# Optimization experiments

Measured on AMD Instinct MI355X. Metric: run time of the kernel, lower is better.

## Reference

```python
import jax, jax.numpy as jnp
import numpy as np

HEADS = 4
OUT_CH = 64
NEG_SLOPE = 0.2  # PyG GATConv default negative_slope


def setup_inputs() -> dict:
    key = jax.random.key(0)
    k1, k2, k3, k4, k5, k6 = jax.random.split(key, 6)
    N, E, IN_CH = 50000, 800000, 128
    x = jax.random.normal(k1, (N, IN_CH), dtype=jnp.float32)
    edge_index = jax.random.randint(k2, (2, E), 0, N, dtype=jnp.int64)
    # Learned parameters (glorot-style init)
    s_w = (6.0 / (IN_CH + HEADS * OUT_CH)) ** 0.5
    W = jax.random.uniform(k3, (IN_CH, HEADS * OUT_CH), minval=-s_w, maxval=s_w, dtype=jnp.float32)
    s_a = (6.0 / (1 + OUT_CH)) ** 0.5
    att_src = jax.random.uniform(k4, (HEADS, OUT_CH), minval=-s_a, maxval=s_a, dtype=jnp.float32)
    att_dst = jax.random.uniform(k5, (HEADS, OUT_CH), minval=-s_a, maxval=s_a, dtype=jnp.float32)
    bias = jnp.zeros((HEADS * OUT_CH,), dtype=jnp.float32)
    return {"x": x, "W": W, "att_src": att_src, "att_dst": att_dst, "bias": bias, "edge_index": edge_index}


def reference(x, W, att_src, att_dst, bias, edge_index):
    # Faithful GATConv (PyG defaults: add_self_loops=True, concat=True, eval mode => no dropout)
    N = x.shape[0]
    loops = jnp.arange(N, dtype=edge_index.dtype)
    src = jnp.concatenate([edge_index[0], loops])  # message source j
    dst = jnp.concatenate([edge_index[1], loops])  # message target i

    xp = (x @ W).reshape(N, HEADS, OUT_CH)          # [N, H, C]
    a_src = jnp.einsum('nhc,hc->nh', xp, att_src)   # [N, H]
    a_dst = jnp.einsum('nhc,hc->nh', xp, att_dst)   # [N, H]

    alpha = jax.nn.leaky_relu(a_src[src] + a_dst[dst], NEG_SLOPE)  # [E', H]
    # segment softmax over incoming edges of each target node
    amax = jax.ops.segment_max(alpha, dst, num_segments=N)
    ex = jnp.exp(alpha - jax.lax.stop_gradient(amax)[dst])
    denom = jax.ops.segment_sum(ex, dst, num_segments=N)
    coef = ex / denom[dst]                           # [E', H]

    msg = xp[src] * coef[:, :, None]                 # [E', H, C]
    out = jax.ops.segment_sum(msg, dst, num_segments=N)  # [N, H, C]
    return out.reshape(N, HEADS * OUT_CH) + bias
```

## Files before the change

kernel.cpp:

```cpp
#include <hip/hip_runtime.h>

#define HEADS 4
#define OUTC 64
#define INC 128
#define HC 256
#define NEG 0.2f

typedef __attribute__((ext_vector_type(8))) short bf16x8;
typedef __attribute__((ext_vector_type(4))) float f32x4;

static __device__ __forceinline__ float bf2f(unsigned short u){
  unsigned int x = ((unsigned int)u) << 16;
  return __uint_as_float(x);
}
static __device__ __forceinline__ unsigned short f2bf(float f){
  unsigned int x = __float_as_uint(f);
  unsigned int lsb = (x >> 16) & 1u;
  x += 0x7fffu + lsb;
  return (unsigned short)(x >> 16);
}
static __device__ __forceinline__ void split8(float4 a, float4 b, bf16x8& hi, bf16x8& lo){
  float v[8] = {a.x, a.y, a.z, a.w, b.x, b.y, b.z, b.w};
  #pragma unroll
  for (int i = 0; i < 8; ++i){
    unsigned short h = f2bf(v[i]);
    hi[i] = (short)h;
    lo[i] = (short)f2bf(v[i] - bf2f(h));
  }
}

__global__ void k_conv_e_hist(const int* __restrict__ ei,
                              int* __restrict__ srcc, int* __restrict__ dstc,
                              int* __restrict__ pos, int* __restrict__ deg, int E){
  int e = blockIdx.x * 256 + threadIdx.x;
  bool valid = (e < E);
  int ee = valid ? e : 0;
  int hiw = ei[2 * ee + 1];
  bool hz = valid ? (hiw == 0) : true;
  unsigned long long mask = __ballot(hz);
  bool i64 = (mask == ~0ULL);
  int s, d;
  if (i64){ s = ei[2 * ee]; d = ei[2 * (size_t)E + 2 * ee]; }
  else    { s = ei[ee];     d = ei[(size_t)E + ee]; }
  if (valid){
    srcc[e] = s; dstc[e] = d;
    pos[e] = atomicAdd(&deg[d], 1);
  }
}

__global__ void k_split_w(const float* __restrict__ W, unsigned short* __restrict__ Wthi,
                          unsigned short* __restrict__ Wtlo){
  int t = blockIdx.x * 256 + threadIdx.x;
  int k = t >> 8, n = t & 255;
  float v = W[t];
  unsigned short hi = f2bf(v);
  Wthi[n * INC + k] = hi;
  Wtlo[n * INC + k] = f2bf(v - bf2f(hi));
}

__global__ __launch_bounds__(256) void k_gemm_fused(const float* __restrict__ X,
    const unsigned short* __restrict__ Wthi, const unsigned short* __restrict__ Wtlo,
    const float* __restrict__ att_src, const float* __restrict__ att_dst,
    unsigned short* __restrict__ XPh, float* __restrict__ a_src, float* __restrict__ a_dst,
    int N){
  int w = threadIdx.x >> 6, lane = threadIdx.x & 63;
  int m0 = blockIdx.x * 64;
  int quad = lane >> 4;
  int l15 = lane & 15;
  int colg[4];
  #pragma unroll
  for (int t = 0; t < 4; ++t) colg[t] = w * 64 + t * 16 + l15;

  bool rv[4]; int rowr[4];
  #pragma unroll
  for (int rt = 0; rt < 4; ++rt){
    rv[rt] = (m0 + rt * 16) < N;
    rowr[rt] = rv[rt] ? (m0 + rt * 16 + l15) : 0;
  }

  f32x4 acc[4][4];
  #pragma unroll
  for (int rt = 0; rt < 4; ++rt)
    #pragma unroll
    for (int t = 0; t < 4; ++t) acc[rt][t] = (f32x4){0.f, 0.f, 0.f, 0.f};

  #pragma unroll
  for (int kk = 0; kk < 4; ++kk){
    float4 va[4], vb[4];
    #pragma unroll
    for (int rt = 0; rt < 4; ++rt){
      const float* xr = X + (size_t)rowr[rt] * INC + kk * 32 + quad * 8;
      va[rt] = *(const float4*)xr;
      vb[rt] = *(const float4*)(xr + 4);
    }
    bf16x8 bh[4], bl[4];
    #pragma unroll
    for (int t = 0; t < 4; ++t){
      size_t bo = (size_t)colg[t] * INC + kk * 32 + quad * 8;
      bh[t] = *(const bf16x8*)(Wthi + bo);
      bl[t] = *(const bf16x8*)(Wtlo + bo);
    }
    bf16x8 ah[4], al[4];
    #pragma unroll
    for (int rt = 0; rt < 4; ++rt) split8(va[rt], vb[rt], ah[rt], al[rt]);
    #pragma unroll
    for (int rt = 0; rt < 4; ++rt){
      #pragma unroll
      for (int t = 0; t < 4; ++t){
        acc[rt][t] = __builtin_amdgcn_mfma_f32_16x16x32_bf16(ah[rt], bh[t], acc[rt][t], 0, 0, 0);
        acc[rt][t] = __builtin_amdgcn_mfma_f32_16x16x32_bf16(ah[rt], bl[t], acc[rt][t], 0, 0, 0);
        acc[rt][t] = __builtin_amdgcn_mfma_f32_16x16x32_bf16(al[rt], bh[t], acc[rt][t], 0, 0, 0);
      }
    }
  }

  #pragma unroll
  for (int rt = 0; rt < 4; ++rt){
    if (!rv[rt]) continue;
    #pragma unroll
    for (int t = 0; t < 4; ++t){
      #pragma unroll
      for (int r = 0; r < 4; ++r){
        XPh[(size_t)(m0 + rt * 16 + quad * 4 + r) * HC + colg[t]] = f2bf(acc[rt][t][r]);
      }
    }
  }

  float as[4], ad[4];
  #pragma unroll
  for (int t = 0; t < 4; ++t){
    as[t] = att_src[colg[t]];
    ad[t] = att_dst[colg[t]];
  }
  #pragma unroll
  for (int rt = 0; rt < 4; ++rt){
    if (!rv[rt]) continue;
    float ps[4], pd[4];
    #pragma unroll
    for (int r = 0; r < 4; ++r){
      ps[r] = acc[rt][0][r] * as[0] + acc[rt][1][r] * as[1]
            + acc[rt][2][r] * as[2] + acc[rt][3][r] * as[3];
      pd[r] = acc[rt][0][r] * ad[0] + acc[rt][1][r] * ad[1]
            + acc[rt][2][r] * ad[2] + acc[rt][3][r] * ad[3];
    }
    #pragma unroll
    for (int msk = 1; msk < 16; msk <<= 1){
      #pragma unroll
      for (int r = 0; r < 4; ++r){
        ps[r] += __shfl_xor(ps[r], msk, 64);
        pd[r] += __shfl_xor(pd[r], msk, 64);
      }
    }
    if (l15 == 0){
      #pragma unroll
      for (int r = 0; r < 4; ++r){
        int n = m0 + rt * 16 + quad * 4 + r;
        a_src[n * HEADS + w] = ps[r];
        a_dst[n * HEADS + w] = pd[r];
      }
    }
  }
}

__global__ __launch_bounds__(256) void k_scan1(const int* __restrict__ deg,
                                               int* __restrict__ out,
                                               int* __restrict__ bsum, int N){
  __shared__ int tsum[256];
  int t = threadIdx.x;
  int base = blockIdx.x * 1024 + t * 4;
  int v[4]; int s = 0;
  #pragma unroll
  for (int k = 0; k < 4; ++k){ int i = base + k; v[k] = (i < N) ? deg[i] : 0; s += v[k]; }
  tsum[t] = s;
  __syncthreads();
  for (int off = 1; off < 256; off <<= 1){
    int x = (t >= off) ? tsum[t - off] : 0;
    __syncthreads();
    tsum[t] += x;
    __syncthreads();
  }
  int excl = tsum[t] - s;
  if (t == 255) bsum[blockIdx.x] = tsum[255];
  int run = excl;
  #pragma unroll
  for (int k = 0; k < 4; ++k){ int i = base + k; if (i < N) out[i] = run; run += v[k]; }
}

__global__ __launch_bounds__(256) void k_scan23(int* __restrict__ rowstart,
                                                const int* __restrict__ bsum,
                                                int N, int E){
  int lane = threadIdx.x & 63;
  int partial = 0;
  for (int i = lane; i < blockIdx.x; i += 64) partial += bsum[i];
  #pragma unroll
  for (int msk = 32; msk; msk >>= 1) partial += __shfl_xor(partial, msk, 64);
  int base = blockIdx.x * 1024 + threadIdx.x * 4;
  #pragma unroll
  for (int k = 0; k < 4; ++k){ int i = base + k; if (i < N) rowstart[i] += partial; }
  if (blockIdx.x == 0 && threadIdx.x == 0) rowstart[N] = E;
}

__global__ void k_scatter(const int* __restrict__ srcc, const int* __restrict__ dstc,
                          const int* __restrict__ pos, const int* __restrict__ rowstart,
                          int* __restrict__ csr, int E){
  int e = blockIdx.x * 256 + threadIdx.x;
  if (e < E){
    int d = dstc[e];
    csr[rowstart[d] + pos[e]] = srcc[e];
  }
}

__global__ __launch_bounds__(256) void k_fused(const unsigned short* __restrict__ XPh,
    const float* __restrict__ a_src, const float* __restrict__ a_dst,
    const int* __restrict__ rowstart, const int* __restrict__ csr,
    const float* __restrict__ bias, float* __restrict__ out, int N){
  __shared__ float sh[4][64][4];
  int w = threadIdx.x >> 6, lane = threadIdx.x & 63;
  int n = blockIdx.x * 4 + w;
  bool alive = (n < N);
  if (!alive) n = 0;
  int r0 = rowstart[n], r1 = rowstart[n + 1];
  int deg = r1 - r0;
  int total = deg + 1;
  int h = lane >> 4;
  float4 ad4 = *(const float4*)&a_dst[n * HEADS];
  bool fast = (total <= 64);
  int jv = n;
  float msel = 0.f, inv_sel = 0.f;

  if (fast){
    if (lane < deg) jv = csr[r0 + lane];
    float l0 = -1e30f, l1 = -1e30f, l2 = -1e30f, l3 = -1e30f;
    if (lane < total){
      float4 a4 = *(const float4*)&a_src[jv * HEADS];
      l0 = a4.x + ad4.x; l0 = (l0 > 0.f) ? l0 : NEG * l0;
      l1 = a4.y + ad4.y; l1 = (l1 > 0.f) ? l1 : NEG * l1;
      l2 = a4.z + ad4.z; l2 = (l2 > 0.f) ? l2 : NEG * l2;
      l3 = a4.w + ad4.w; l3 = (l3 > 0.f) ? l3 : NEG * l3;
    }
    float p0 = __expf(l0), p1 = __expf(l1), p2 = __expf(l2), p3 = __expf(l3);
    float s0 = p0, s1 = p1, s2 = p2, s3 = p3;
    #pragma unroll
    for (int msk = 32; msk; msk >>= 1){
      s0 += __shfl_xor(s0, msk, 64);
      s1 += __shfl_xor(s1, msk, 64);
      s2 += __shfl_xor(s2, msk, 64);
      s3 += __shfl_xor(s3, msk, 64);
    }
    if (lane < total){
      sh[w][lane][0] = p0 / s0;
      sh[w][lane][1] = p1 / s1;
      sh[w][lane][2] = p2 / s2;
      sh[w][lane][3] = p3 / s3;
    }
  } else {
    float m[4] = {-1e30f, -1e30f, -1e30f, -1e30f};
    float s[4] = {0.f, 0.f, 0.f, 0.f};
    float adArr[4] = {ad4.x, ad4.y, ad4.z, ad4.w};
    for (int e = lane; e < total; e += 64){
      int j = (e < deg) ? csr[r0 + e] : n;
      float4 a4 = *(const float4*)&a_src[j * HEADS];
      float aa[4] = {a4.x, a4.y, a4.z, a4.w};
      #pragma unroll
      for (int hh = 0; hh < 4; ++hh){
        float l = aa[hh] + adArr[hh];
        l = (l > 0.f) ? l : NEG * l;
        if (l > m[hh]){ s[hh] = s[hh] * __expf(m[hh] - l) + 1.f; m[hh] = l; }
        else            s[hh] += __expf(l - m[hh]);
      }
    }
    #pragma unroll
    for (int hh = 0; hh < 4; ++hh){
      float mm = m[hh], ss = s[hh];
      #pragma unroll
      for (int msk = 32; msk; msk >>= 1){
        float m2 = __shfl_xor(mm, msk, 64);
        float s2 = __shfl_xor(ss, msk, 64);
        float M = fmaxf(mm, m2);
        float ns = 0.f;
        if (mm > -1e29f) ns += ss * __expf(mm - M);
        if (m2 > -1e29f) ns += s2 * __expf(m2 - M);
        mm = M; ss = ns;
      }
      m[hh] = mm; s[hh] = ss;
    }
    msel    = (h == 0) ? m[0] : (h == 1) ? m[1] : (h == 2) ? m[2] : m[3];
    inv_sel = 1.f / ((h == 0) ? s[0] : (h == 1) ? s[1] : (h == 2) ? s[2] : s[3]);
  }

  __syncthreads();

  float a0 = 0.f, a1 = 0.f, a2 = 0.f, a3 = 0.f;
  const unsigned short* xb = XPh + lane * 4;
  if (fast){
    int e = 0;
    for (; e + 8 <= total; e += 8){
      int jj[8]; float cf[8]; ushort4 xv[8];
      #pragma unroll
      for (int q = 0; q < 8; ++q){
        jj[q] = __builtin_amdgcn_readlane(jv, e + q);
        cf[q] = sh[w][e + q][h];
      }
      #pragma unroll
      for (int q = 0; q < 8; ++q) xv[q] = *(const ushort4*)(xb + (size_t)jj[q] * HC);
      #pragma unroll
      for (int q = 0; q < 8; ++q){
        a0 += cf[q] * bf2f(xv[q].x); a1 += cf[q] * bf2f(xv[q].y);
        a2 += cf[q] * bf2f(xv[q].z); a3 += cf[q] * bf2f(xv[q].w);
      }
    }
    for (; e < total; ++e){
      int j = __builtin_amdgcn_readlane(jv, e);
      float c = sh[w][e][h];
      ushort4 xv = *(const ushort4*)(xb + (size_t)j * HC);
      a0 += c * bf2f(xv.x); a1 += c * bf2f(xv.y); a2 += c * bf2f(xv.z); a3 += c * bf2f(xv.w);
    }
  } else {
    float adh = (h == 0) ? ad4.x : (h == 1) ? ad4.y : (h == 2) ? ad4.z : ad4.w;
    for (int e = 0; e < total; ++e){
      int j = (e < deg) ? csr[r0 + e] : n;
      float4 a4 = *(const float4*)&a_src[j * HEADS];
      float ah = (h == 0) ? a4.x : (h == 1) ? a4.y : (h == 2) ? a4.z : a4.w;
      float l = ah + adh;
      l = (l > 0.f) ? l : NEG * l;
      float c = __expf(l - msel) * inv_sel;
      ushort4 xv = *(const ushort4*)(xb + (size_t)j * HC);
      a0 += c * bf2f(xv.x); a1 += c * bf2f(xv.y); a2 += c * bf2f(xv.z); a3 += c * bf2f(xv.w);
    }
  }
  if (alive){
    float4 b4 = *(const float4*)&bias[lane * 4];
    float4 r; r.x = a0 + b4.x; r.y = a1 + b4.y; r.z = a2 + b4.z; r.w = a3 + b4.w;
    *(float4*)&out[(size_t)n * HC + lane * 4] = r;
  }
}

extern "C" void kernel_launch(void* const* d_in, const int* in_sizes, int n_in,
                              void* d_out, int out_size, void* d_ws, size_t ws_size,
                              hipStream_t stream){
  const float* x       = (const float*)d_in[0];
  const float* W       = (const float*)d_in[1];
  const float* att_src = (const float*)d_in[2];
  const float* att_dst = (const float*)d_in[3];
  const float* bias    = (const float*)d_in[4];
  const int*   ei      = (const int*)d_in[5];
  int N = in_sizes[0] / INC;
  int E = in_sizes[5] / 2;

  char* p = (char*)d_ws;
  auto alloc = [&](size_t bytes)->char*{
    char* r = p; p += (bytes + 255) & ~(size_t)255; return r;
  };
  unsigned short* Wthi = (unsigned short*)alloc((size_t)INC * HC * 2);
  unsigned short* Wtlo = (unsigned short*)alloc((size_t)INC * HC * 2);
  unsigned short* XPh  = (unsigned short*)alloc((size_t)N * HC * 2);
  float* aSrc          = (float*)alloc((size_t)N * HEADS * 4);
  float* aDst          = (float*)alloc((size_t)N * HEADS * 4);
  int* deg             = (int*)alloc((size_t)N * 4);
  int* rowstart        = (int*)alloc(((size_t)N + 1) * 4);
  int* srcc            = (int*)alloc((size_t)E * 4);
  int* dstc            = (int*)alloc((size_t)E * 4);
  int* pos             = (int*)alloc((size_t)E * 4);
  int* csr             = (int*)alloc((size_t)E * 4);
  int* bsum            = (int*)alloc(256 * 4);

  hipMemsetAsync(deg, 0, (size_t)N * 4, stream);
  k_conv_e_hist<<<(E + 255) / 256, 256, 0, stream>>>(ei, srcc, dstc, pos, deg, E);

  k_split_w<<<(INC * HC) / 256, 256, 0, stream>>>(W, Wthi, Wtlo);
  k_gemm_fused<<<(N + 63) / 64, 256, 0, stream>>>(x, Wthi, Wtlo, att_src, att_dst,
                                                  XPh, aSrc, aDst, N);

  int nb = (N + 1023) / 1024;
  k_scan1<<<nb, 256, 0, stream>>>(deg, rowstart, bsum, N);
  k_scan23<<<nb, 256, 0, stream>>>(rowstart, bsum, N, E);
  k_scatter<<<(E + 255) / 256, 256, 0, stream>>>(srcc, dstc, pos, rowstart, csr, E);

  k_fused<<<(N + 3) / 4, 256, 0, stream>>>(XPh, aSrc, aDst, rowstart, csr, bias,
                                           (float*)d_out, N);
}
```

Measured before the change: 249.4 us.

## Merge preprocessing kernels, share split X tiles via LDS, use nontemporal output stores

Folds the W split kernel and the edge conversion/histogram kernel into one launch, which saves a kernel launch. In the GEMM, each wave now loads and splits only its own 16 rows of X and shares the bf16 hi/lo parts through LDS. Previously every wave redundantly loaded and split all 64 rows, so this trades redundant global loads and conversion ALU work for extra barriers. It also drops a __syncthreads in the aggregation kernel and writes the output with nontemporal stores to avoid polluting the cache.

```diff
diff --git a/kernel.cpp b/kernel.cpp
--- a/kernel.cpp
+++ b/kernel.cpp
@@ -29,10 +29,22 @@
   }
 }
 
-__global__ void k_conv_e_hist(const int* __restrict__ ei,
-                              int* __restrict__ srcc, int* __restrict__ dstc,
-                              int* __restrict__ pos, int* __restrict__ deg, int E){
-  int e = blockIdx.x * 256 + threadIdx.x;
+#define SPLITB 128
+
+__global__ void k_pre(const float* __restrict__ W, unsigned short* __restrict__ Wthi,
+                      unsigned short* __restrict__ Wtlo, const int* __restrict__ ei,
+                      int* __restrict__ srcc, int* __restrict__ dstc,
+                      int* __restrict__ pos, int* __restrict__ deg, int E){
+  if (blockIdx.x < SPLITB){
+    int t = blockIdx.x * 256 + threadIdx.x;
+    int k = t >> 8, n = t & 255;
+    float v = W[t];
+    unsigned short hi = f2bf(v);
+    Wthi[n * INC + k] = hi;
+    Wtlo[n * INC + k] = f2bf(v - bf2f(hi));
+    return;
+  }
+  int e = (blockIdx.x - SPLITB) * 256 + threadIdx.x;
   bool valid = (e < E);
   int ee = valid ? e : 0;
   int hiw = ei[2 * ee + 1];
@@ -48,21 +60,13 @@
   }
 }
 
-__global__ void k_split_w(const float* __restrict__ W, unsigned short* __restrict__ Wthi,
-                          unsigned short* __restrict__ Wtlo){
-  int t = blockIdx.x * 256 + threadIdx.x;
-  int k = t >> 8, n = t & 255;
-  float v = W[t];
-  unsigned short hi = f2bf(v);
-  Wthi[n * INC + k] = hi;
-  Wtlo[n * INC + k] = f2bf(v - bf2f(hi));
-}
-
 __global__ __launch_bounds__(256) void k_gemm_fused(const float* __restrict__ X,
     const unsigned short* __restrict__ Wthi, const unsigned short* __restrict__ Wtlo,
     const float* __restrict__ att_src, const float* __restrict__ att_dst,
     unsigned short* __restrict__ XPh, float* __restrict__ a_src, float* __restrict__ a_dst,
     int N){
+  __shared__ unsigned short shi[64][40];
+  __shared__ unsigned short slo[64][40];
   int w = threadIdx.x >> 6, lane = threadIdx.x & 63;
   int m0 = blockIdx.x * 64;
   int quad = lane >> 4;
@@ -71,12 +75,10 @@
   #pragma unroll
   for (int t = 0; t < 4; ++t) colg[t] = w * 64 + t * 16 + l15;
 
-  bool rv[4]; int rowr[4];
-  #pragma unroll
-  for (int rt = 0; rt < 4; ++rt){
-    rv[rt] = (m0 + rt * 16) < N;
-    rowr[rt] = rv[rt] ? (m0 + rt * 16 + l15) : 0;
-  }
+  bool rv[4];
+  #pragma unroll
+  for (int rt = 0; rt < 4; ++rt) rv[rt] = (m0 + rt * 16) < N;
+  int myrow = rv[w] ? (m0 + w * 16 + l15) : 0;
 
   f32x4 acc[4][4];
   #pragma unroll
@@ -86,13 +88,9 @@
 
   #pragma unroll
   for (int kk = 0; kk < 4; ++kk){
-    float4 va[4], vb[4];
-    #pragma unroll
-    for (int rt = 0; rt < 4; ++rt){
-      const float* xr = X + (size_t)rowr[rt] * INC + kk * 32 + quad * 8;
-      va[rt] = *(const float4*)xr;
-      vb[rt] = *(const float4*)(xr + 4);
-    }
+    const float* xr = X + (size_t)myrow * INC + kk * 32 + quad * 8;
+    float4 va = *(const float4*)xr;
+    float4 vb = *(const float4*)(xr + 4);
     bf16x8 bh[4], bl[4];
     #pragma unroll
     for (int t = 0; t < 4; ++t){
@@ -100,9 +98,18 @@
       bh[t] = *(const bf16x8*)(Wthi + bo);
       bl[t] = *(const bf16x8*)(Wtlo + bo);
     }
+    bf16x8 ah1, al1;
+    split8(va, vb, ah1, al1);
+    if (kk) __syncthreads();
+    *(bf16x8*)&shi[w * 16 + l15][quad * 8] = ah1;
+    *(bf16x8*)&slo[w * 16 + l15][quad * 8] = al1;
+    __syncthreads();
     bf16x8 ah[4], al[4];
     #pragma unroll
-    for (int rt = 0; rt < 4; ++rt) split8(va[rt], vb[rt], ah[rt], al[rt]);
+    for (int rt = 0; rt < 4; ++rt){
+      ah[rt] = *(const bf16x8*)&shi[rt * 16 + l15][quad * 8];
+      al[rt] = *(const bf16x8*)&slo[rt * 16 + l15][quad * 8];
+    }
     #pragma unroll
     for (int rt = 0; rt < 4; ++rt){
       #pragma unroll
@@ -288,8 +295,6 @@
     inv_sel = 1.f / ((h == 0) ? s[0] : (h == 1) ? s[1] : (h == 2) ? s[2] : s[3]);
   }
 
-  __syncthreads();
-
   float a0 = 0.f, a1 = 0.f, a2 = 0.f, a3 = 0.f;
   const unsigned short* xb = XPh + lane * 4;
   if (fast){
@@ -330,8 +335,9 @@
   }
   if (alive){
     float4 b4 = *(const float4*)&bias[lane * 4];
-    float4 r; r.x = a0 + b4.x; r.y = a1 + b4.y; r.z = a2 + b4.z; r.w = a3 + b4.w;
-    *(float4*)&out[(size_t)n * HC + lane * 4] = r;
+    f32x4 r;
+    r[0] = a0 + b4.x; r[1] = a1 + b4.y; r[2] = a2 + b4.z; r[3] = a3 + b4.w;
+    __builtin_nontemporal_store(r, (f32x4*)&out[(size_t)n * HC + lane * 4]);
   }
 }
 
@@ -365,9 +371,8 @@
   int* bsum            = (int*)alloc(256 * 4);
 
   hipMemsetAsync(deg, 0, (size_t)N * 4, stream);
-  k_conv_e_hist<<<(E + 255) / 256, 256, 0, stream>>>(ei, srcc, dstc, pos, deg, E);
-
-  k_split_w<<<(INC * HC) / 256, 256, 0, stream>>>(W, Wthi, Wtlo);
+  k_pre<<<SPLITB + (E + 255) / 256, 256, 0, stream>>>(W, Wthi, Wtlo, ei,
+                                                      srcc, dstc, pos, deg, E);
   k_gemm_fused<<<(N + 63) / 64, 256, 0, stream>>>(x, Wthi, Wtlo, att_src, att_dst,
                                                   XPh, aSrc, aDst, N);
 
```

Measured after the change: 238.1 us. 4.5% less time.
